# Optimization experiments

Hardware: AMD Instinct MI355X
Metric: run time of the kernel (lower is better)

Reference implementation:

```python
import jax, jax.numpy as jnp
import numpy as np

K = 1024   # number of NNLS components (theta_1 is K x K)
B = 8192   # batched frames / columns


def setup_inputs() -> dict:
    key = jax.random.key(0)
    k1, k2, k3, k4 = jax.random.split(key, 4)
    # theta_1 = I - AtA / ||AtA||_F  -> near-identity contraction; emulate with
    # identity minus a small random symmetric-ish perturbation.
    pert = jax.random.normal(k1, (K, K), dtype=jnp.float32) * (1.0 / K)
    th1 = jnp.eye(K, dtype=jnp.float32) - pert
    Y = jax.random.uniform(k2, (K, B), dtype=jnp.float32)
    X_old = jax.random.uniform(k3, (K, B), dtype=jnp.float32)
    weight = jax.random.normal(k4, (K, B), dtype=jnp.float32) * 0.1  # theta_2 = Atb/n_AtA
    k = 2  # PGD iteration counter
    return {"th1": th1, "Y": Y, "X_old": X_old, "k": k, "weight": weight}


def reference(th1, Y, X_old, k, weight):
    # One projected-gradient-descent step of NNLS with Nesterov momentum:
    #   new_X = relu(th1 @ Y + weight)
    #   Y_new = new_X + (k-1)/(k+2) * (new_X - X_old)
    kf = jnp.float32(k)
    new_X = jax.nn.relu(jnp.matmul(th1, Y) + weight)          # [K, B]
    momentum = (kf - 1.0) / (kf + 2.0)
    Y_new = new_X + momentum * (new_X - X_old)                # [K, B]
    return (Y_new, new_X, k + 1, weight)
```

## Files before the change

### kernel.cpp

```cpp
#include <hip/hip_runtime.h>
#include <cstdint>


#define KDIM 1024
#define NDIM 8192
#define KB_ELEMS (1024UL * 8192UL)
#define YT_BYTES (8192UL * 1024UL * 2UL)
#define AB_BYTES (1024UL * 1024UL * 2UL)
#define WS_NEED (YT_BYTES + AB_BYTES)

typedef short short8 __attribute__((ext_vector_type(8)));
typedef float f32x4 __attribute__((ext_vector_type(4)));

struct __attribute__((aligned(4))) f4u { float x, y, z, w; };

__device__ __forceinline__ uint32_t pk2(float a, float b) {
  uint32_t ua = __builtin_bit_cast(uint32_t, a) + 0x8000u;
  uint32_t ub = __builtin_bit_cast(uint32_t, b) + 0x8000u;
  return (ua >> 16) | (ub & 0xFFFF0000u);
}

__device__ __forceinline__ void ldsload16(const void* g, void* l) {
  __builtin_amdgcn_global_load_lds(
      (const __attribute__((address_space(1))) uint32_t*)g,
      (__attribute__((address_space(3))) uint32_t*)l, 16, 0, 0);
}

__global__ __launch_bounds__(256) void nnls_conv(
    const float* __restrict__ th1, const float* __restrict__ Y,
    char* __restrict__ ws)
{
  unsigned short* yt  = (unsigned short*)ws;
  unsigned short* abf = (unsigned short*)(ws + YT_BYTES);
  const int tid = threadIdx.x;
  if (blockIdx.x < 1024) {
    const int kt = blockIdx.x >> 5;
    const int nb = blockIdx.x & 31;
    const int k0 = kt * 32, n0 = nb * 256;
    __shared__ float t[32][260];
#pragma unroll
    for (int it = 0; it < 8; ++it) {
      const int r = it * 4 + (tid >> 6);
      const float4 v = *(const float4*)&Y[(size_t)(k0 + r) * NDIM + n0 + (tid & 63) * 4];
      *(float4*)&t[r][(tid & 63) * 4] = v;
    }
    __syncthreads();
    const int n = tid;
    __attribute__((aligned(16))) uint32_t o[16];
#pragma unroll
    for (int r2 = 0; r2 < 16; ++r2) o[r2] = pk2(t[2 * r2][n], t[2 * r2 + 1][n]);
    uint32_t* dst = (uint32_t*)&yt[((size_t)kt * NDIM + (n0 + n)) * 32];
#pragma unroll
    for (int q = 0; q < 4; ++q) *(uint4*)&dst[q * 4] = *(uint4*)&o[q * 4];
  } else {
    const int id = (blockIdx.x - 1024) * 256 + tid;
    const int m = id >> 5, kt = id & 31;
    const float4* s4 = (const float4*)(th1 + (size_t)m * KDIM + kt * 32);
    __attribute__((aligned(16))) uint32_t o[16];
#pragma unroll
    for (int q = 0; q < 8; ++q) {
      const float4 v = s4[q];
      o[2 * q]     = pk2(v.x, v.y);
      o[2 * q + 1] = pk2(v.z, v.w);
    }
    uint32_t* dst = (uint32_t*)&abf[((size_t)kt * KDIM + m) * 32];
#pragma unroll
    for (int q = 0; q < 4; ++q) *(uint4*)&dst[q * 4] = *(uint4*)&o[q * 4];
  }
}

__global__ __launch_bounds__(256, 4) void nnls_gemm2(
    const char* __restrict__ ws, const float* __restrict__ xold,
    const int* __restrict__ kin, const float* __restrict__ weight,
    float* __restrict__ out)
{
  const char* yt = ws;
  const char* ab = ws + YT_BYTES;
  __shared__ __align__(16) char smem[24576];

  const int tid  = threadIdx.x;
  const int lane = tid & 63;
  const int w    = tid >> 6;
  const int wm = w >> 1, wn = w & 1;
  const int quad = lane >> 4, nl = lane & 15;

  const int m0 = blockIdx.y * 128;
  const int n0 = blockIdx.x * 64;

  const char* ag = ab + (size_t)m0 * 64 + w * 2048 + lane * 16;
  const char* bg = yt + (size_t)n0 * 64 + w * 1024 + lane * 16;

  f32x4 acc[4][2] = {};

  {
    char* buf = smem;
    ldsload16(ag,        buf + w * 2048);
    ldsload16(ag + 1024, buf + w * 2048 + 1024);
    ldsload16(bg,        buf + 8192 + w * 1024);
  }
  __syncthreads();

#pragma unroll 2
  for (int kt = 0; kt < 32; ++kt) {
    char* cur = smem + (kt & 1) * 12288;
    char* nxt = smem + ((kt & 1) ^ 1) * 12288;
    if (kt < 31) {
      const char* a2 = ag + (size_t)(kt + 1) * 65536;
      const char* b2 = bg + (size_t)(kt + 1) * 524288;
      ldsload16(a2,        nxt + w * 2048);
      ldsload16(a2 + 1024, nxt + w * 2048 + 1024);
      ldsload16(b2,        nxt + 8192 + w * 1024);
    }
    const unsigned short* Asp = (const unsigned short*)cur;
    const unsigned short* Bsp = (const unsigned short*)(cur + 8192);
    short8 af[4], bf[2];
#pragma unroll
    for (int i = 0; i < 4; ++i)
      af[i] = *(const short8*)&Asp[(wm * 64 + i * 16 + nl) * 32 + quad * 8];
#pragma unroll
    for (int j = 0; j < 2; ++j)
      bf[j] = *(const short8*)&Bsp[(wn * 32 + j * 16 + nl) * 32 + quad * 8];
#pragma unroll
    for (int i = 0; i < 4; ++i)
#pragma unroll
      for (int j = 0; j < 2; ++j)
        acc[i][j] = __builtin_amdgcn_mfma_f32_16x16x32_bf16(af[i], bf[j], acc[i][j], 0, 0, 0);
    __syncthreads();
  }

  const float kf  = (float)kin[0];
  const float mom = (kf - 1.0f) / (kf + 2.0f);
  float* ep = (float*)(smem + w * 2304);
  const int rl = lane >> 3;
  const int cq = lane & 7;

#pragma unroll
  for (int i = 0; i < 4; ++i) {
#pragma unroll
    for (int j = 0; j < 2; ++j)
#pragma unroll
      for (int r = 0; r < 4; ++r)
        ep[(quad * 4 + r) * 36 + (j * 16 + nl)] = acc[i][j][r];

    const int mgb = m0 + wm * 64 + i * 16;
#pragma unroll
    for (int t = 0; t < 2; ++t) {
      const int row = t * 8 + rl;
      const float4 cv = *(const float4*)&ep[row * 36 + cq * 4];
      const int ng = n0 + wn * 32 + cq * 4;
      const size_t idx = (size_t)(mgb + row) * NDIM + ng;
      const float4 wv = *(const float4*)&weight[idx];
      const float4 xo = *(const float4*)&xold[idx];
      float4 nx, yn;
      nx.x = fmaxf(cv.x + wv.x, 0.0f); nx.y = fmaxf(cv.y + wv.y, 0.0f);
      nx.z = fmaxf(cv.z + wv.z, 0.0f); nx.w = fmaxf(cv.w + wv.w, 0.0f);
      yn.x = nx.x + mom * (nx.x - xo.x); yn.y = nx.y + mom * (nx.y - xo.y);
      yn.z = nx.z + mom * (nx.z - xo.z); yn.w = nx.w + mom * (nx.w - xo.w);
      *(float4*)&out[idx] = yn;
      *(float4*)&out[KB_ELEMS + idx] = nx;
      f4u s; s.x = wv.x; s.y = wv.y; s.z = wv.z; s.w = wv.w;
      *(f4u*)&out[2 * KB_ELEMS + 1 + idx] = s;
    }
  }

  if (blockIdx.x == 0 && blockIdx.y == 0 && tid == 0)
    out[2 * KB_ELEMS] = (float)(kin[0] + 1);
}

#define LDA 40
__global__ __launch_bounds__(512, 4) void nnls_gemm_v1(
    const float* __restrict__ th1, const float* __restrict__ Y,
    const float* __restrict__ xold, const int* __restrict__ kin,
    const float* __restrict__ weight, float* __restrict__ out)
{
  __shared__ __align__(16) char smem[40960];
  unsigned short* As0 = (unsigned short*)smem;
  unsigned short* Bs0 = (unsigned short*)(smem + 10240);
  unsigned short* As1 = (unsigned short*)(smem + 20480);
  unsigned short* Bs1 = (unsigned short*)(smem + 30720);

  const int tid  = threadIdx.x;
  const int lane = tid & 63;
  const int w    = tid >> 6;
  const int wm = w >> 1, wn = w & 1;
  const int quad = lane >> 4, nl = lane & 15;
  const int m0 = blockIdx.y * 128;
  const int n0 = blockIdx.x * 128;
  const int ar = tid >> 3;
  const int ac = tid & 7;
  const float* abase = th1 + (size_t)(m0 + ar) * KDIM + ac * 4;
  const int bn = tid & 127;
  const int bk = (tid >> 7) * 8;
  const float* ybase = Y + (size_t)bk * NDIM + n0 + bn;

  float4 abv[2];
  float  yb[8];
  abv[0] = *(const float4*)(abase);
  abv[1] = *(const float4*)(abase + (size_t)64 * KDIM);
#pragma unroll
  for (int r = 0; r < 8; ++r) yb[r] = ybase[(size_t)r * NDIM];

  f32x4 acc[2][4] = {};

#pragma unroll 2
  for (int kt = 0; kt < 32; ++kt) {
    unsigned short* Asp = (kt & 1) ? As1 : As0;
    unsigned short* Bsp = (kt & 1) ? Bs1 : Bs0;
    {
      uint2 d0; d0.x = pk2(abv[0].x, abv[0].y); d0.y = pk2(abv[0].z, abv[0].w);
      *(uint2*)&Asp[ar * LDA + ac * 4] = d0;
      uint2 d1; d1.x = pk2(abv[1].x, abv[1].y); d1.y = pk2(abv[1].z, abv[1].w);
      *(uint2*)&Asp[(ar + 64) * LDA + ac * 4] = d1;
      uint4 e;
      e.x = pk2(yb[0], yb[1]); e.y = pk2(yb[2], yb[3]);
      e.z = pk2(yb[4], yb[5]); e.w = pk2(yb[6], yb[7]);
      *(uint4*)&Bsp[bn * LDA + bk] = e;
    }
    __syncthreads();
    if (kt < 31) {
      const float* an = abase + (kt + 1) * 32;
      abv[0] = *(const float4*)(an);
      abv[1] = *(const float4*)(an + (size_t)64 * KDIM);
      const float* yn = ybase + (size_t)((kt + 1) * 32) * NDIM;
#pragma unroll
      for (int r = 0; r < 8; ++r) yb[r] = yn[(size_t)r * NDIM];
    }
    short8 af[2], bf[4];
#pragma unroll
    for (int i = 0; i < 2; ++i)
      af[i] = *(const short8*)&Asp[(wm * 32 + i * 16 + nl) * LDA + quad * 8];
#pragma unroll
    for (int j = 0; j < 4; ++j)
      bf[j] = *(const short8*)&Bsp[(wn * 64 + j * 16 + nl) * LDA + quad * 8];
#pragma unroll
    for (int i = 0; i < 2; ++i)
#pragma unroll
      for (int j = 0; j < 4; ++j)
        acc[i][j] = __builtin_amdgcn_mfma_f32_16x16x32_bf16(af[i], bf[j], acc[i][j], 0, 0, 0);
    __syncthreads();
  }
  __syncthreads();

  const float kf  = (float)kin[0];
  const float mom = (kf - 1.0f) / (kf + 2.0f);
  float* ep = (float*)smem + w * 1088;
  const int u  = lane >> 4;
  const int mc = lane & 15;
#pragma unroll
  for (int i = 0; i < 2; ++i) {
#pragma unroll
    for (int j = 0; j < 4; ++j)
#pragma unroll
      for (int r = 0; r < 4; ++r)
        ep[(quad * 4 + r) * 68 + (j * 16 + nl)] = acc[i][j][r];
    const int mgb = m0 + wm * 32 + i * 16;
#pragma unroll
    for (int t = 0; t < 4; ++t) {
      const int row = t * 4 + u;
      const float4 cv = *(const float4*)&ep[row * 68 + mc * 4];
      const int ng = n0 + wn * 64 + mc * 4;
      const size_t idx = (size_t)(mgb + row) * NDIM + ng;
      const float4 wv = *(const float4*)&weight[idx];
      const float4 xo = *(const float4*)&xold[idx];
      float4 nx, yn;
      nx.x = fmaxf(cv.x + wv.x, 0.0f); nx.y = fmaxf(cv.y + wv.y, 0.0f);
      nx.z = fmaxf(cv.z + wv.z, 0.0f); nx.w = fmaxf(cv.w + wv.w, 0.0f);
      yn.x = nx.x + mom * (nx.x - xo.x); yn.y = nx.y + mom * (nx.y - xo.y);
      yn.z = nx.z + mom * (nx.z - xo.z); yn.w = nx.w + mom * (nx.w - xo.w);
      *(float4*)&out[idx] = yn;
      *(float4*)&out[KB_ELEMS + idx] = nx;
      f4u s; s.x = wv.x; s.y = wv.y; s.z = wv.z; s.w = wv.w;
      *(f4u*)&out[2 * KB_ELEMS + 1 + idx] = s;
    }
  }
  if (blockIdx.x == 0 && blockIdx.y == 0 && tid == 0)
    out[2 * KB_ELEMS] = (float)(kin[0] + 1);
}

extern "C" void kernel_launch(void* const* d_in, const int* in_sizes, int n_in,
                              void* d_out, int out_size, void* d_ws, size_t ws_size,
                              hipStream_t stream) {
  const float* th1  = (const float*)d_in[0];
  const float* Y    = (const float*)d_in[1];
  const float* xold = (const float*)d_in[2];
  const int*   kin  = (const int*)d_in[3];
  const float* wgt  = (const float*)d_in[4];
  float* out = (float*)d_out;

  if (d_ws != nullptr && ws_size >= WS_NEED) {
    nnls_conv<<<1152, 256, 0, stream>>>(th1, Y, (char*)d_ws);
    nnls_gemm2<<<dim3(NDIM / 64, KDIM / 128), 256, 0, stream>>>(
        (const char*)d_ws, xold, kin, wgt, out);
  } else {
    nnls_gemm_v1<<<dim3(NDIM / 128, KDIM / 128), 512, 0, stream>>>(
        th1, Y, xold, kin, wgt, out);
  }
}
```

Baseline: 226.5 us.

## Swizzle bf16 workspace layout and use 2-wave blocks with larger per-wave tiles

The conversion kernel now reads Y directly per column without an LDS transpose and writes the bf16 chunks with an XOR swizzle. The th1 conversion is remapped so consecutive threads cover consecutive rows. The GEMM kernel halves the block to 128 threads, and each wave computes a 64x64 tile (4x4 MFMA accumulators) using swizzled LDS fragment reads to avoid bank conflicts. The epilogue prefetches weight and x_old before staging results through LDS. This trades higher register use and lower occupancy for more MFMA work per LDS fragment load and fewer LDS conflicts.

```diff
diff --git a/kernel.cpp b/kernel.cpp
--- a/kernel.cpp
+++ b/kernel.cpp
@@ -35,26 +35,22 @@
   const int tid = threadIdx.x;
   if (blockIdx.x < 1024) {
     const int kt = blockIdx.x >> 5;
-    const int nb = blockIdx.x & 31;
-    const int k0 = kt * 32, n0 = nb * 256;
-    __shared__ float t[32][260];
-#pragma unroll
-    for (int it = 0; it < 8; ++it) {
-      const int r = it * 4 + (tid >> 6);
-      const float4 v = *(const float4*)&Y[(size_t)(k0 + r) * NDIM + n0 + (tid & 63) * 4];
-      *(float4*)&t[r][(tid & 63) * 4] = v;
-    }
-    __syncthreads();
-    const int n = tid;
+    const int n  = (blockIdx.x & 31) * 256 + tid;
+    const float* src = Y + (size_t)kt * 32 * NDIM + n;
+    float v[32];
+#pragma unroll
+    for (int r = 0; r < 32; ++r) v[r] = src[(size_t)r * NDIM];
     __attribute__((aligned(16))) uint32_t o[16];
 #pragma unroll
-    for (int r2 = 0; r2 < 16; ++r2) o[r2] = pk2(t[2 * r2][n], t[2 * r2 + 1][n]);
-    uint32_t* dst = (uint32_t*)&yt[((size_t)kt * NDIM + (n0 + n)) * 32];
-#pragma unroll
-    for (int q = 0; q < 4; ++q) *(uint4*)&dst[q * 4] = *(uint4*)&o[q * 4];
+    for (int r = 0; r < 16; ++r) o[r] = pk2(v[2 * r], v[2 * r + 1]);
+    const int perm = (n >> 1) & 3;
+    uint4* dst = (uint4*)(yt + ((size_t)kt * NDIM + n) * 32);
+    const uint4* o4 = (const uint4*)o;
+#pragma unroll
+    for (int q = 0; q < 4; ++q) dst[q ^ perm] = o4[q];
   } else {
     const int id = (blockIdx.x - 1024) * 256 + tid;
-    const int m = id >> 5, kt = id & 31;
+    const int kt = id >> 10, m = id & 1023;
     const float4* s4 = (const float4*)(th1 + (size_t)m * KDIM + kt * 32);
     __attribute__((aligned(16))) uint32_t o[16];
 #pragma unroll
@@ -63,13 +59,15 @@
       o[2 * q]     = pk2(v.x, v.y);
       o[2 * q + 1] = pk2(v.z, v.w);
     }
-    uint32_t* dst = (uint32_t*)&abf[((size_t)kt * KDIM + m) * 32];
-#pragma unroll
-    for (int q = 0; q < 4; ++q) *(uint4*)&dst[q * 4] = *(uint4*)&o[q * 4];
-  }
-}
-
-__global__ __launch_bounds__(256, 4) void nnls_gemm2(
+    const int perm = (m >> 1) & 3;
+    uint4* dst = (uint4*)(abf + ((size_t)kt * KDIM + m) * 32);
+    const uint4* o4 = (const uint4*)o;
+#pragma unroll
+    for (int q = 0; q < 4; ++q) dst[q ^ perm] = o4[q];
+  }
+}
+
+__global__ __launch_bounds__(128, 2) void nnls_gemm3(
     const char* __restrict__ ws, const float* __restrict__ xold,
     const int* __restrict__ kin, const float* __restrict__ weight,
     float* __restrict__ out)
@@ -81,24 +79,25 @@
   const int tid  = threadIdx.x;
   const int lane = tid & 63;
   const int w    = tid >> 6;
-  const int wm = w >> 1, wn = w & 1;
   const int quad = lane >> 4, nl = lane & 15;
 
   const int m0 = blockIdx.y * 128;
   const int n0 = blockIdx.x * 64;
 
-  const char* ag = ab + (size_t)m0 * 64 + w * 2048 + lane * 16;
-  const char* bg = yt + (size_t)n0 * 64 + w * 1024 + lane * 16;
-
-  f32x4 acc[4][2] = {};
+  const char* ag = ab + (size_t)m0 * 64 + w * 4096 + lane * 16;
+  const char* bg = yt + (size_t)n0 * 64 + w * 2048 + lane * 16;
+
+  f32x4 acc[4][4] = {};
 
   {
-    char* buf = smem;
-    ldsload16(ag,        buf + w * 2048);
-    ldsload16(ag + 1024, buf + w * 2048 + 1024);
-    ldsload16(bg,        buf + 8192 + w * 1024);
+#pragma unroll
+    for (int q = 0; q < 4; ++q) ldsload16(ag + q * 1024, smem + w * 4096 + q * 1024);
+#pragma unroll
+    for (int q = 0; q < 2; ++q) ldsload16(bg + q * 1024, smem + 8192 + w * 2048 + q * 1024);
   }
   __syncthreads();
+
+  const int fro = (quad ^ ((nl >> 1) & 3)) * 8;
 
 #pragma unroll 2
   for (int kt = 0; kt < 32; ++kt) {
@@ -107,58 +106,61 @@
     if (kt < 31) {
       const char* a2 = ag + (size_t)(kt + 1) * 65536;
       const char* b2 = bg + (size_t)(kt + 1) * 524288;
-      ldsload16(a2,        nxt + w * 2048);
-      ldsload16(a2 + 1024, nxt + w * 2048 + 1024);
-      ldsload16(b2,        nxt + 8192 + w * 1024);
+#pragma unroll
+      for (int q = 0; q < 4; ++q) ldsload16(a2 + q * 1024, nxt + w * 4096 + q * 1024);
+#pragma unroll
+      for (int q = 0; q < 2; ++q) ldsload16(b2 + q * 1024, nxt + 8192 + w * 2048 + q * 1024);
     }
     const unsigned short* Asp = (const unsigned short*)cur;
     const unsigned short* Bsp = (const unsigned short*)(cur + 8192);
-    short8 af[4], bf[2];
+    short8 af[4], bf[4];
 #pragma unroll
     for (int i = 0; i < 4; ++i)
-      af[i] = *(const short8*)&Asp[(wm * 64 + i * 16 + nl) * 32 + quad * 8];
-#pragma unroll
-    for (int j = 0; j < 2; ++j)
-      bf[j] = *(const short8*)&Bsp[(wn * 32 + j * 16 + nl) * 32 + quad * 8];
+      af[i] = *(const short8*)&Asp[(w * 64 + i * 16 + nl) * 32 + fro];
+#pragma unroll
+    for (int j = 0; j < 4; ++j)
+      bf[j] = *(const short8*)&Bsp[(j * 16 + nl) * 32 + fro];
 #pragma unroll
     for (int i = 0; i < 4; ++i)
 #pragma unroll
-      for (int j = 0; j < 2; ++j)
+      for (int j = 0; j < 4; ++j)
         acc[i][j] = __builtin_amdgcn_mfma_f32_16x16x32_bf16(af[i], bf[j], acc[i][j], 0, 0, 0);
     __syncthreads();
   }
 
   const float kf  = (float)kin[0];
   const float mom = (kf - 1.0f) / (kf + 2.0f);
-  float* ep = (float*)(smem + w * 2304);
-  const int rl = lane >> 3;
-  const int cq = lane & 7;
+  float* ep = (float*)(smem + w * 4608);
+  const int u  = lane >> 4;
+  const int cq = lane & 15;
 
 #pragma unroll
   for (int i = 0; i < 4; ++i) {
-#pragma unroll
-    for (int j = 0; j < 2; ++j)
+    const int mgb = m0 + w * 64 + i * 16;
+    size_t idxs[4]; float4 wv[4], xo[4];
+#pragma unroll
+    for (int t = 0; t < 4; ++t) {
+      idxs[t] = (size_t)(mgb + t * 4 + u) * NDIM + n0 + cq * 4;
+      wv[t] = *(const float4*)&weight[idxs[t]];
+      xo[t] = *(const float4*)&xold[idxs[t]];
+    }
+#pragma unroll
+    for (int j = 0; j < 4; ++j)
 #pragma unroll
       for (int r = 0; r < 4; ++r)
-        ep[(quad * 4 + r) * 36 + (j * 16 + nl)] = acc[i][j][r];
-
-    const int mgb = m0 + wm * 64 + i * 16;
-#pragma unroll
-    for (int t = 0; t < 2; ++t) {
-      const int row = t * 8 + rl;
-      const float4 cv = *(const float4*)&ep[row * 36 + cq * 4];
-      const int ng = n0 + wn * 32 + cq * 4;
-      const size_t idx = (size_t)(mgb + row) * NDIM + ng;
-      const float4 wv = *(const float4*)&weight[idx];
-      const float4 xo = *(const float4*)&xold[idx];
+        ep[(quad * 4 + r) * 68 + j * 16 + nl] = acc[i][j][r];
+#pragma unroll
+    for (int t = 0; t < 4; ++t) {
+      const float4 cv = *(const float4*)&ep[(t * 4 + u) * 68 + cq * 4];
+      const size_t idx = idxs[t];
       float4 nx, yn;
-      nx.x = fmaxf(cv.x + wv.x, 0.0f); nx.y = fmaxf(cv.y + wv.y, 0.0f);
-      nx.z = fmaxf(cv.z + wv.z, 0.0f); nx.w = fmaxf(cv.w + wv.w, 0.0f);
-      yn.x = nx.x + mom * (nx.x - xo.x); yn.y = nx.y + mom * (nx.y - xo.y);
-      yn.z = nx.z + mom * (nx.z - xo.z); yn.w = nx.w + mom * (nx.w - xo.w);
+      nx.x = fmaxf(cv.x + wv[t].x, 0.0f); nx.y = fmaxf(cv.y + wv[t].y, 0.0f);
+      nx.z = fmaxf(cv.z + wv[t].z, 0.0f); nx.w = fmaxf(cv.w + wv[t].w, 0.0f);
+      yn.x = nx.x + mom * (nx.x - xo[t].x); yn.y = nx.y + mom * (nx.y - xo[t].y);
+      yn.z = nx.z + mom * (nx.z - xo[t].z); yn.w = nx.w + mom * (nx.w - xo[t].w);
       *(float4*)&out[idx] = yn;
       *(float4*)&out[KB_ELEMS + idx] = nx;
-      f4u s; s.x = wv.x; s.y = wv.y; s.z = wv.z; s.w = wv.w;
+      f4u s; s.x = wv[t].x; s.y = wv[t].y; s.z = wv[t].z; s.w = wv[t].w;
       *(f4u*)&out[2 * KB_ELEMS + 1 + idx] = s;
     }
   }
@@ -289,7 +291,7 @@
 
   if (d_ws != nullptr && ws_size >= WS_NEED) {
     nnls_conv<<<1152, 256, 0, stream>>>(th1, Y, (char*)d_ws);
-    nnls_gemm2<<<dim3(NDIM / 64, KDIM / 128), 256, 0, stream>>>(
+    nnls_gemm3<<<dim3(NDIM / 64, KDIM / 128), 128, 0, stream>>>(
         (const char*)d_ws, xold, kin, wgt, out);
   } else {
     nnls_gemm_v1<<<dim3(NDIM / 128, KDIM / 128), 512, 0, stream>>>(
```

Result: no change. 230.3 us (+1.7%).
